# Performance work log

Measured on AMD Instinct MI355X. Metric: run time of the kernel, lower is better.

Reference implementation:

```python
import jax, jax.numpy as jnp
import numpy as np

NUM_HEADS = 16

def rotate_half(x):
    x1, x2 = jnp.split(x, 2, axis=-1)
    return jnp.concatenate([-x2, x1], axis=-1)

def setup_inputs() -> dict:
    key = jax.random.key(0)
    ks = jax.random.split(key, 12)
    B, S, D = 2, 2048, 1024
    sc = 1.0 / np.sqrt(D)
    return {
        "x": jax.random.normal(ks[0], (B, S, D), dtype=jnp.float32),
        "cdr_mask": jax.random.uniform(ks[1], (B, 1, S, S), dtype=jnp.float32),
        "Wq": jax.random.normal(ks[2], (D, D), dtype=jnp.float32) * sc,
        "bq": jnp.zeros((D,), dtype=jnp.float32),
        "Wk": jax.random.normal(ks[3], (D, D), dtype=jnp.float32) * sc,
        "bk": jnp.zeros((D,), dtype=jnp.float32),
        "Wv": jax.random.normal(ks[4], (D, D), dtype=jnp.float32) * sc,
        "bv": jnp.zeros((D,), dtype=jnp.float32),
        "Wo": jax.random.normal(ks[5], (D, D), dtype=jnp.float32) * sc,
        "bo": jnp.zeros((D,), dtype=jnp.float32),
        "cdr_weight": jnp.asarray(1.0, dtype=jnp.float32),
    }

def reference(x, cdr_mask, Wq, bq, Wk, bk, Wv, bv, Wo, bo, cdr_weight):
    B, S, D = x.shape
    H = NUM_HEADS
    hd = D // H
    # RoPE tables: NOTE original uses full head_dim frequencies (not head_dim/2)
    inv_freq = 1.0 / (10000.0 ** (jnp.arange(hd, dtype=jnp.float32) / hd))
    pos = jnp.arange(S, dtype=jnp.float32)
    sinusoid = pos[:, None] * inv_freq[None, :]          # [S, hd]
    sin_pos = jnp.sin(sinusoid)[None, None]              # [1,1,S,hd]
    cos_pos = jnp.cos(sinusoid)[None, None]

    def heads(y):  # [B,S,D] -> [B,H,S,hd]
        return y.reshape(B, S, H, hd).transpose(0, 2, 1, 3)

    Q = heads(x @ Wq + bq)
    K = heads(x @ Wk + bk)
    V = heads(x @ Wv + bv)
    Qr = Q * cos_pos + rotate_half(Q) * sin_pos
    Kr = K * cos_pos + rotate_half(K) * sin_pos

    scores = jnp.einsum('bhqd,bhkd->bhqk', Qr, Kr) / jnp.sqrt(jnp.asarray(hd, x.dtype))
    scores = scores * (1.0 + cdr_mask * cdr_weight)      # multiplicative learned mask
    attn = jax.nn.softmax(scores, axis=-1)               # dropout is identity in eval
    out = jnp.einsum('bhqk,bhkd->bhqd', attn, V)
    out = out.transpose(0, 2, 1, 3).reshape(B, S, D)
    return out @ Wo + bo
```

## Files before the change

kernel.cpp:

```cpp
#include <hip/hip_runtime.h>
#include <stdint.h>

typedef unsigned short u16;
typedef __bf16 bf16x8 __attribute__((ext_vector_type(8)));
typedef float f32x4 __attribute__((ext_vector_type(4)));
typedef float fx4 __attribute__((ext_vector_type(4)));
typedef unsigned short u16x8 __attribute__((ext_vector_type(8)));
typedef unsigned short u16x4 __attribute__((ext_vector_type(4)));

#define DEV __device__ __forceinline__

DEV u16 f2bf(float f) {
  unsigned u = __builtin_bit_cast(unsigned, f);
  u += 0x7fff + ((u >> 16) & 1);
  return (u16)(u >> 16);
}

DEV f32x4 mfma16(bf16x8 a, bf16x8 b, f32x4 c) {
  return __builtin_amdgcn_mfma_f32_16x16x32_bf16(a, b, c, 0, 0, 0);
}

DEV void gload16(const void* g, void* l) {
  __builtin_amdgcn_global_load_lds(
      (const __attribute__((address_space(1))) unsigned int*)g,
      (__attribute__((address_space(3))) unsigned int*)l, 16, 0, 0);
}

__global__ __launch_bounds__(256) void k_tables(float* __restrict__ cosT,
                                                float* __restrict__ sinT) {
  int i = blockIdx.x * 256 + threadIdx.x;
  int s = i >> 6, d = i & 63;
  float inv = exp2f(-(float)d * (13.287712379549449f / 64.f));
  float a = (float)s * inv;
  cosT[i] = cosf(a);
  sinT[i] = sinf(a);
}

__global__ __launch_bounds__(256) void k_cvt(const float* __restrict__ x,
                                             u16* __restrict__ xb) {
  int i = (blockIdx.x * 256 + threadIdx.x) * 4;
  fx4 f = *reinterpret_cast<const fx4*>(x + i);
  u16x4 o;
#pragma unroll
  for (int j = 0; j < 4; ++j) o[j] = f2bf(f[j]);
  *reinterpret_cast<u16x4*>(xb + i) = o;
}

__global__ __launch_bounds__(256) void k_wtrans(
    const float* __restrict__ W0, const float* __restrict__ W1,
    const float* __restrict__ W2, const float* __restrict__ W3,
    u16* __restrict__ O0, u16* __restrict__ O1,
    u16* __restrict__ O2, u16* __restrict__ O3) {
  __shared__ u16 T[64][66];
  const float* W = (blockIdx.z == 0) ? W0 : (blockIdx.z == 1) ? W1
                   : (blockIdx.z == 2) ? W2 : W3;
  u16* O = (blockIdx.z == 0) ? O0 : (blockIdx.z == 1) ? O1
           : (blockIdx.z == 2) ? O2 : O3;
  const int t = threadIdx.x;
  const int k0 = blockIdx.y * 64, n0 = blockIdx.x * 64;
  const int r = t >> 2, cc = (t & 3) * 16;
  const float* src = W + (long)(k0 + r) * 1024 + n0 + cc;
#pragma unroll
  for (int u = 0; u < 16; u += 4) {
    fx4 f = *reinterpret_cast<const fx4*>(src + u);
#pragma unroll
    for (int j = 0; j < 4; ++j) T[r][cc + u + j] = f2bf(f[j]);
  }
  __syncthreads();
  const int n = t >> 2, kc = (t & 3) * 16;
  u16x8 o1, o2;
#pragma unroll
  for (int j = 0; j < 8; ++j) { o1[j] = T[kc + j][n]; o2[j] = T[kc + 8 + j][n]; }
  u16* dst = O + (long)(n0 + n) * 1024 + k0 + kc;
  *reinterpret_cast<u16x8*>(dst) = o1;
  *reinterpret_cast<u16x8*>(dst + 8) = o2;
}

__global__ __launch_bounds__(256) void k_gemm_qkv(
    const u16* __restrict__ A, const u16* __restrict__ Bt,
    const float* __restrict__ bq, const float* __restrict__ bk,
    const float* __restrict__ bv, const float* __restrict__ cosT,
    const float* __restrict__ sinT, u16* __restrict__ qb,
    u16* __restrict__ kb, u16* __restrict__ vb) {
  __shared__ u16 As[128 * 32];
  __shared__ u16 Bs[128 * 32];
  const int t = threadIdx.x;
  const int lane = t & 63, wid = t >> 6;
  const int wm = wid >> 1, wn = wid & 1;
  const int l15 = lane & 15, lg = lane >> 4;
  const int bm = blockIdx.x, bn = blockIdx.y;

  f32x4 acc[4][4];
#pragma unroll
  for (int m = 0; m < 4; ++m)
#pragma unroll
    for (int n = 0; n < 4; ++n) acc[m][n] = f32x4{0.f, 0.f, 0.f, 0.f};

  const int arow = t >> 2;
  const int acol = (t & 3) << 3;
  const u16* Ab = A + (long)(bm * 128 + arow) * 1024 + acol;
  const u16* Bb = Bt + (long)(bn * 128 + arow) * 1024 + acol;

  for (int k0 = 0; k0 < 1024; k0 += 32) {
    gload16(Ab + k0, As + t * 8);
    gload16(Ab + 64 * 1024 + k0, As + 2048 + t * 8);
    gload16(Bb + k0, Bs + t * 8);
    gload16(Bb + 64 * 1024 + k0, Bs + 2048 + t * 8);
    __syncthreads();
    bf16x8 af[4], bfr[4];
#pragma unroll
    for (int m = 0; m < 4; ++m)
      af[m] = *reinterpret_cast<const bf16x8*>(As + (wm * 64 + m * 16 + l15) * 32 + lg * 8);
#pragma unroll
    for (int n = 0; n < 4; ++n)
      bfr[n] = *reinterpret_cast<const bf16x8*>(Bs + (wn * 64 + n * 16 + l15) * 32 + lg * 8);
#pragma unroll
    for (int m = 0; m < 4; ++m)
#pragma unroll
      for (int n = 0; n < 4; ++n) acc[m][n] = mfma16(af[m], bfr[n], acc[m][n]);
    __syncthreads();
  }

  const int seg = bn >> 3;
  const float* bias = (seg == 0) ? bq : (seg == 1) ? bk : bv;
  u16* outb = (seg == 0) ? qb : (seg == 1) ? kb : vb;
  const int h = (bn & 7) * 2 + wn;
#pragma unroll
  for (int m = 0; m < 4; ++m) {
#pragma unroll
    for (int reg = 0; reg < 4; ++reg) {
      const int rg = bm * 128 + wm * 64 + m * 16 + lg * 4 + reg;
      const int s = rg & 2047, b = rg >> 11;
      float v4[4];
#pragma unroll
      for (int n = 0; n < 4; ++n)
        v4[n] = acc[m][n][reg] + bias[(bn & 7) * 128 + wn * 64 + n * 16 + l15];
      if (seg < 2) {
#pragma unroll
        for (int n = 0; n < 4; ++n) {
          const int d = n * 16 + l15;
          float c = cosT[s * 64 + d], sn = sinT[s * 64 + d];
          float rot = (n < 2) ? -v4[n + 2] : v4[n - 2];
          outb[((long)(b * 16 + h) * 2048 + s) * 64 + d] = f2bf(v4[n] * c + rot * sn);
        }
      } else {
#pragma unroll
        for (int n = 0; n < 4; ++n)
          outb[((long)(b * 16 + h) * 2048 + s) * 64 + n * 16 + l15] = f2bf(v4[n]);
      }
    }
  }
}

__global__ __launch_bounds__(256) void k_gemm_out(
    const u16* __restrict__ A, const u16* __restrict__ Bt,
    const float* __restrict__ bias, float* __restrict__ outf) {
  __shared__ u16 As[128 * 32];
  __shared__ u16 Bs[128 * 32];
  const int t = threadIdx.x;
  const int lane = t & 63, wid = t >> 6;
  const int wm = wid >> 1, wn = wid & 1;
  const int l15 = lane & 15, lg = lane >> 4;
  const int bm = blockIdx.x, bn = blockIdx.y;

  f32x4 acc[4][4];
#pragma unroll
  for (int m = 0; m < 4; ++m)
#pragma unroll
    for (int n = 0; n < 4; ++n) acc[m][n] = f32x4{0.f, 0.f, 0.f, 0.f};

  const int arow = t >> 2;
  const int acol = (t & 3) << 3;
  const u16* Ab = A + (long)(bm * 128 + arow) * 1024 + acol;
  const u16* Bb = Bt + (long)(bn * 128 + arow) * 1024 + acol;

  for (int k0 = 0; k0 < 1024; k0 += 32) {
    gload16(Ab + k0, As + t * 8);
    gload16(Ab + 64 * 1024 + k0, As + 2048 + t * 8);
    gload16(Bb + k0, Bs + t * 8);
    gload16(Bb + 64 * 1024 + k0, Bs + 2048 + t * 8);
    __syncthreads();
    bf16x8 af[4], bfr[4];
#pragma unroll
    for (int m = 0; m < 4; ++m)
      af[m] = *reinterpret_cast<const bf16x8*>(As + (wm * 64 + m * 16 + l15) * 32 + lg * 8);
#pragma unroll
    for (int n = 0; n < 4; ++n)
      bfr[n] = *reinterpret_cast<const bf16x8*>(Bs + (wn * 64 + n * 16 + l15) * 32 + lg * 8);
#pragma unroll
    for (int m = 0; m < 4; ++m)
#pragma unroll
      for (int n = 0; n < 4; ++n) acc[m][n] = mfma16(af[m], bfr[n], acc[m][n]);
    __syncthreads();
  }

#pragma unroll
  for (int m = 0; m < 4; ++m)
#pragma unroll
    for (int reg = 0; reg < 4; ++reg) {
      const int rg = bm * 128 + wm * 64 + m * 16 + lg * 4 + reg;
#pragma unroll
      for (int n = 0; n < 4; ++n)
        outf[(long)rg * 1024 + bn * 128 + wn * 64 + n * 16 + l15] =
            acc[m][n][reg] + bias[bn * 128 + wn * 64 + n * 16 + l15];
    }
}

__global__ __launch_bounds__(256) void k_vtrans(const u16* __restrict__ VB,
                                                u16* __restrict__ VT) {
  __shared__ u16 T[64][66];
  const int t = threadIdx.x;
  const int bh = blockIdx.y;
  const int s0 = blockIdx.x * 64;
  const int r = t >> 2, c = (t & 3) * 16;
  const u16* src = VB + ((long)bh * 2048 + s0 + r) * 64 + c;
  u16x8 a = *reinterpret_cast<const u16x8*>(src);
  u16x8 b = *reinterpret_cast<const u16x8*>(src + 8);
#pragma unroll
  for (int j = 0; j < 8; ++j) { T[r][c + j] = a[j]; T[r][c + 8 + j] = b[j]; }
  __syncthreads();
  const int d = t >> 2, sc = (t & 3) * 16;
  u16x8 o1, o2;
#pragma unroll
  for (int j = 0; j < 8; ++j) { o1[j] = T[sc + j][d]; o2[j] = T[sc + 8 + j][d]; }
  u16* dst = VT + ((long)bh * 64 + d) * 2048 + s0 + sc;
  *reinterpret_cast<u16x8*>(dst) = o1;
  *reinterpret_cast<u16x8*>(dst + 8) = o2;
}

__global__ __launch_bounds__(256, 2) void k_attn(
    const u16* __restrict__ Qb, const u16* __restrict__ Kb,
    const u16* __restrict__ Vt, const float* __restrict__ mask,
    const float* __restrict__ wp, u16* __restrict__ Ob) {
  __shared__ u16 Ks[2][64 * 64];
  __shared__ u16 Vs[2][64 * 64];
  __shared__ u16 Ps[4][32 * 64];
  const int t = threadIdx.x, lane = t & 63, wid = t >> 6;
  const int l15 = lane & 15, lg = lane >> 4;
  const int b = blockIdx.z, hh = blockIdx.y;
  const int bh = b * 16 + hh;
  const int qw = blockIdx.x * 128 + wid * 32;
  const float c1 = 0.18033688f;
  const float c2 = c1 * wp[0];

  bf16x8 qf[2][2];
#pragma unroll
  for (int m = 0; m < 2; ++m) {
    const u16* Qrow = Qb + ((long)bh * 2048 + qw + m * 16 + l15) * 64 + lg * 8;
    qf[m][0] = *reinterpret_cast<const bf16x8*>(Qrow);
    qf[m][1] = *reinterpret_cast<const bf16x8*>(Qrow + 32);
  }

  bf16x8 ones;
#pragma unroll
  for (int j = 0; j < 8; ++j) ones[j] = (__bf16)1.0f;

  f32x4 oacc[2][4];
#pragma unroll
  for (int m = 0; m < 2; ++m)
#pragma unroll
    for (int n = 0; n < 4; ++n) oacc[m][n] = f32x4{0.f, 0.f, 0.f, 0.f};
  f32x4 lsum[2] = {f32x4{0.f, 0.f, 0.f, 0.f}, f32x4{0.f, 0.f, 0.f, 0.f}};

  const u16* Kbase = Kb + (long)bh * 2048 * 64;
  const u16* Vbase = Vt + (long)bh * 64 * 2048;
  const float* Mbase = mask + (long)b * 2048 * 2048 + (long)(qw + lg * 4) * 2048 + l15;

  const int krow = t >> 3;
  const int kcs = ((t & 7) * 8) ^ ((krow & 7) << 3);

#define STAGE(buf, kt)                                                       \
  do {                                                                       \
    gload16(Kbase + (long)((kt) + krow) * 64 + kcs, Ks[buf] + t * 8);        \
    gload16(Kbase + (long)((kt) + krow + 32) * 64 + kcs,                     \
            Ks[buf] + 2048 + t * 8);                                         \
    gload16(Vbase + (long)krow * 2048 + (kt) + kcs, Vs[buf] + t * 8);        \
    gload16(Vbase + (long)(krow + 32) * 2048 + (kt) + kcs,                   \
            Vs[buf] + 2048 + t * 8);                                         \
  } while (0)

  STAGE(0, 0);
  __syncthreads();
  int cur = 0;

  for (int kt = 0; kt < 2048; kt += 64) {
    if (kt + 64 < 2048) STAGE(cur ^ 1, kt + 64);

    float mv[2][4][4];
#pragma unroll
    for (int m = 0; m < 2; ++m)
#pragma unroll
      for (int reg = 0; reg < 4; ++reg)
#pragma unroll
        for (int n = 0; n < 4; ++n)
          mv[m][reg][n] = Mbase[(long)(m * 16 + reg) * 2048 + kt + n * 16];

    f32x4 sc[2][4];
#pragma unroll
    for (int m = 0; m < 2; ++m)
#pragma unroll
      for (int n = 0; n < 4; ++n) sc[m][n] = f32x4{0.f, 0.f, 0.f, 0.f};
#pragma unroll
    for (int ks = 0; ks < 2; ++ks) {
      const int ko = (ks * 32 + lg * 8) ^ ((l15 & 7) << 3);
      bf16x8 kf[4];
#pragma unroll
      for (int n = 0; n < 4; ++n)
        kf[n] = *reinterpret_cast<const bf16x8*>(Ks[cur] + (n * 16 + l15) * 64 + ko);
#pragma unroll
      for (int m = 0; m < 2; ++m)
#pragma unroll
        for (int n = 0; n < 4; ++n) sc[m][n] = mfma16(qf[m][ks], kf[n], sc[m][n]);
    }

#pragma unroll
    for (int m = 0; m < 2; ++m)
#pragma unroll
      for (int n = 0; n < 4; ++n)
#pragma unroll
        for (int reg = 0; reg < 4; ++reg) {
          float mult = __builtin_fmaf(mv[m][reg][n], c2, c1);
          float p = exp2f(sc[m][n][reg] * mult);
          const int r = m * 16 + lg * 4 + reg;
          Ps[wid][r * 64 + ((n * 16 + l15) ^ ((r & 7) << 3))] =
              __builtin_bit_cast(u16, (__bf16)p);
        }

#pragma unroll
    for (int ks = 0; ks < 2; ++ks) {
      const int ko = (ks * 32 + lg * 8) ^ ((l15 & 7) << 3);
      bf16x8 pf[2];
      pf[0] = *reinterpret_cast<const bf16x8*>(Ps[wid] + l15 * 64 + ko);
      pf[1] = *reinterpret_cast<const bf16x8*>(Ps[wid] + (16 + l15) * 64 + ko);
      lsum[0] = mfma16(pf[0], ones, lsum[0]);
      lsum[1] = mfma16(pf[1], ones, lsum[1]);
#pragma unroll
      for (int n = 0; n < 4; ++n) {
        bf16x8 vf = *reinterpret_cast<const bf16x8*>(Vs[cur] + (n * 16 + l15) * 64 + ko);
        oacc[0][n] = mfma16(pf[0], vf, oacc[0][n]);
        oacc[1][n] = mfma16(pf[1], vf, oacc[1][n]);
      }
    }
    __syncthreads();
    cur ^= 1;
  }
#undef STAGE

#pragma unroll
  for (int m = 0; m < 2; ++m)
#pragma unroll
    for (int n = 0; n < 4; ++n)
#pragma unroll
      for (int reg = 0; reg < 4; ++reg) {
        float v = oacc[m][n][reg] / lsum[m][reg];
        Ob[((long)b * 2048 + qw + m * 16 + lg * 4 + reg) * 1024 + hh * 64 + n * 16 + l15] =
            f2bf(v);
      }
}

extern "C" void kernel_launch(void* const* d_in, const int* in_sizes, int n_in,
                              void* d_out, int out_size, void* d_ws, size_t ws_size,
                              hipStream_t stream) {
  const float* x  = (const float*)d_in[0];
  const float* cm = (const float*)d_in[1];
  const float* Wq = (const float*)d_in[2];
  const float* bq = (const float*)d_in[3];
  const float* Wk = (const float*)d_in[4];
  const float* bk = (const float*)d_in[5];
  const float* Wv = (const float*)d_in[6];
  const float* bv = (const float*)d_in[7];
  const float* Wo = (const float*)d_in[8];
  const float* bo = (const float*)d_in[9];
  const float* cw = (const float*)d_in[10];
  float* out = (float*)d_out;

  char* ws = (char*)d_ws;
  float* cosT = (float*)(ws + 0);
  float* sinT = (float*)(ws + (512u << 10));
  u16* xb  = (u16*)(ws + (1u << 20));
  u16* wqT = (u16*)(ws + (9u << 20));
  u16* woT = (u16*)(ws + (15u << 20));
  u16* qb  = (u16*)(ws + (17u << 20));
  u16* kb  = (u16*)(ws + (25u << 20));
  u16* vb  = (u16*)(ws + (33u << 20));
  u16* vt  = (u16*)(ws + (41u << 20));
  u16* ob  = (u16*)(ws + (49u << 20));
  u16* wkT = wqT + (1u << 20);
  u16* wvT = wqT + (2u << 20);

  k_tables<<<512, 256, 0, stream>>>(cosT, sinT);
  k_cvt<<<4096, 256, 0, stream>>>(x, xb);
  k_wtrans<<<dim3(16, 16, 4), 256, 0, stream>>>(Wq, Wk, Wv, Wo, wqT, wkT, wvT, woT);
  k_gemm_qkv<<<dim3(32, 24), 256, 0, stream>>>(xb, wqT, bq, bk, bv, cosT, sinT, qb, kb, vb);
  k_vtrans<<<dim3(32, 32), 256, 0, stream>>>(vb, vt);
  k_attn<<<dim3(16, 16, 2), 256, 0, stream>>>(qb, kb, vt, cm, cw, ob);
  k_gemm_out<<<dim3(32, 8), 256, 0, stream>>>(ob, woT, bo, out);
}
```

Before: 262.8 us.

## Split attention over key halves with atomic partial accumulation and normalize pass

```diff
diff --git a/kernel.cpp b/kernel.cpp
--- a/kernel.cpp
+++ b/kernel.cpp
@@ -228,18 +228,22 @@
   *reinterpret_cast<u16x8*>(dst + 8) = o2;
 }
 
-__global__ __launch_bounds__(256, 2) void k_attn(
+#define PO_CHUNK 131072
+__global__ __launch_bounds__(256, 3) void k_attn(
     const u16* __restrict__ Qb, const u16* __restrict__ Kb,
     const u16* __restrict__ Vt, const float* __restrict__ mask,
-    const float* __restrict__ wp, u16* __restrict__ Ob) {
+    const float* __restrict__ wp, float* __restrict__ poA,
+    float* __restrict__ poB, float* __restrict__ pl) {
   __shared__ u16 Ks[2][64 * 64];
   __shared__ u16 Vs[2][64 * 64];
   __shared__ u16 Ps[4][32 * 64];
   const int t = threadIdx.x, lane = t & 63, wid = t >> 6;
   const int l15 = lane & 15, lg = lane >> 4;
-  const int b = blockIdx.z, hh = blockIdx.y;
+  const int b = blockIdx.z >> 1, ksh = blockIdx.z & 1;
+  const int hh = blockIdx.y;
   const int bh = b * 16 + hh;
   const int qw = blockIdx.x * 128 + wid * 32;
+  const int kbase = ksh * 1024;
   const float c1 = 0.18033688f;
   const float c2 = c1 * wp[0];
 
@@ -279,12 +283,12 @@
             Vs[buf] + 2048 + t * 8);                                         \
   } while (0)
 
-  STAGE(0, 0);
+  STAGE(0, kbase);
   __syncthreads();
   int cur = 0;
 
-  for (int kt = 0; kt < 2048; kt += 64) {
-    if (kt + 64 < 2048) STAGE(cur ^ 1, kt + 64);
+  for (int kt = kbase; kt < kbase + 1024; kt += 64) {
+    if (kt + 64 < kbase + 1024) STAGE(cur ^ 1, kt + 64);
 
     float mv[2][4][4];
 #pragma unroll
@@ -346,16 +350,41 @@
   }
 #undef STAGE
 
-#pragma unroll
-  for (int m = 0; m < 2; ++m)
+  float* po = (bh < 28) ? (poA + (long)bh * PO_CHUNK)
+                        : (poB + (long)(bh - 28) * PO_CHUNK);
+#pragma unroll
+  for (int m = 0; m < 2; ++m) {
 #pragma unroll
     for (int n = 0; n < 4; ++n)
 #pragma unroll
-      for (int reg = 0; reg < 4; ++reg) {
-        float v = oacc[m][n][reg] / lsum[m][reg];
-        Ob[((long)b * 2048 + qw + m * 16 + lg * 4 + reg) * 1024 + hh * 64 + n * 16 + l15] =
-            f2bf(v);
-      }
+      for (int reg = 0; reg < 4; ++reg)
+        atomicAdd(&po[(qw + m * 16 + lg * 4 + reg) * 64 + n * 16 + l15],
+                  oacc[m][n][reg]);
+    if (l15 == 0) {
+#pragma unroll
+      for (int reg = 0; reg < 4; ++reg)
+        atomicAdd(&pl[bh * 2048 + qw + m * 16 + lg * 4 + reg], lsum[m][reg]);
+    }
+  }
+}
+
+__global__ __launch_bounds__(256) void k_norm(const float* __restrict__ poA,
+                                              const float* __restrict__ poB,
+                                              const float* __restrict__ pl,
+                                              u16* __restrict__ ob) {
+  const long j = ((long)blockIdx.x * 256 + threadIdx.x) * 4;
+  const int bh = (int)(j >> 17);
+  const int q = (int)(j >> 6) & 2047;
+  const int d = (int)j & 63;
+  const float* po = (bh < 28) ? (poA + (long)bh * PO_CHUNK)
+                              : (poB + (long)(bh - 28) * PO_CHUNK);
+  fx4 v = *reinterpret_cast<const fx4*>(&po[q * 64 + d]);
+  const float inv = 1.0f / pl[bh * 2048 + q];
+  const int b = bh >> 4, hh = bh & 15;
+  u16x4 o;
+#pragma unroll
+  for (int i = 0; i < 4; ++i) o[i] = f2bf(v[i] * inv);
+  *reinterpret_cast<u16x4*>(&ob[((long)(b * 2048 + q)) * 1024 + hh * 64 + d]) = o;
 }
 
 extern "C" void kernel_launch(void* const* d_in, const int* in_sizes, int n_in,
@@ -388,11 +417,18 @@
   u16* wkT = wqT + (1u << 20);
   u16* wvT = wqT + (2u << 20);
 
+  float* poA = (float*)(ws + 0);
+  float* pl  = (float*)(ws + 14680064u);
+  float* poB = (float*)(ws + (33u << 20));
+
   k_tables<<<512, 256, 0, stream>>>(cosT, sinT);
   k_cvt<<<4096, 256, 0, stream>>>(x, xb);
   k_wtrans<<<dim3(16, 16, 4), 256, 0, stream>>>(Wq, Wk, Wv, Wo, wqT, wkT, wvT, woT);
   k_gemm_qkv<<<dim3(32, 24), 256, 0, stream>>>(xb, wqT, bq, bk, bv, cosT, sinT, qb, kb, vb);
+  hipMemsetAsync(ws, 0, 14680064u + 262144u, stream);
   k_vtrans<<<dim3(32, 32), 256, 0, stream>>>(vb, vt);
-  k_attn<<<dim3(16, 16, 2), 256, 0, stream>>>(qb, kb, vt, cm, cw, ob);
+  hipMemsetAsync(ws + (33u << 20), 0, 4u * PO_CHUNK * sizeof(float), stream);
+  k_attn<<<dim3(16, 16, 4), 256, 0, stream>>>(qb, kb, vt, cm, cw, poA, poB, pl);
+  k_norm<<<4096, 256, 0, stream>>>(poA, poB, pl, ob);
   k_gemm_out<<<dim3(32, 8), 256, 0, stream>>>(ob, woT, bo, out);
 }
```

Result: slower. 315.0 us (+19.9%).
